# Kernel optimization log

Measured on AMD Instinct MI355X. Metric: run time of the kernel, lower is better.

## Reference

```python
import jax, jax.numpy as jnp
import numpy as np

N = 20000       # nodes
E = 640000      # edges (before self-loops)
F_IN = 128      # num_features
H = 128         # hidden channels (both GAT layers)
C = 40          # num_classes
NEG_SLOPE = 0.2  # PyG GATConv default


def _glorot(key, shape):
    fan = sum(shape)
    return jax.random.normal(key, shape, dtype=jnp.float32) * jnp.sqrt(2.0 / fan)


def setup_inputs() -> dict:
    key = jax.random.key(0)
    ks = jax.random.split(key, 12)
    x = jax.random.normal(ks[0], (N, F_IN), dtype=jnp.float32)
    edge_index = jax.random.randint(ks[1], (2, E), 0, N, dtype=jnp.int64)
    return {
        "x": x,
        "edge_index": edge_index,
        # GATConv layer 1 (heads=1): lin weight, att_src, att_dst, bias
        "W1": _glorot(ks[2], (F_IN, H)),
        "a1_src": _glorot(ks[3], (H,)),
        "a1_dst": _glorot(ks[4], (H,)),
        "b1": jnp.zeros((H,), dtype=jnp.float32),
        # GATConv layer 2
        "W2": _glorot(ks[5], (H, H)),
        "a2_src": _glorot(ks[6], (H,)),
        "a2_dst": _glorot(ks[7], (H,)),
        "b2": jnp.zeros((H,), dtype=jnp.float32),
        # final linear classifier
        "Wl": _glorot(ks[8], (H, C)),
        "bl": jnp.zeros((C,), dtype=jnp.float32),
    }


def gat_conv(x, src, dst, W, a_src, a_dst, b):
    """PyG GATConv, heads=1, concat=True, negative_slope=0.2 (self-loops already in edge list)."""
    h = x @ W                                   # [N, H]
    alpha_src = h @ a_src                       # [N]
    alpha_dst = h @ a_dst                       # [N]
    e = jax.nn.leaky_relu(alpha_src[src] + alpha_dst[dst], NEG_SLOPE)  # [E']
    # numerically stable softmax over incoming edges per destination node
    m = jax.ops.segment_max(e, dst, num_segments=N)        # [N]
    ex = jnp.exp(e - m[dst])                                # [E']
    den = jax.ops.segment_sum(ex, dst, num_segments=N)      # [N]
    alpha = ex / den[dst]                                   # [E']
    out = jax.ops.segment_sum(h[src] * alpha[:, None], dst, num_segments=N)  # [N, H]
    return out + b


def reference(x, edge_index, W1, a1_src, a1_dst, b1, W2, a2_src, a2_dst, b2, Wl, bl):
    # GATConv adds self-loops by default
    loops = jnp.arange(N, dtype=edge_index.dtype)
    src = jnp.concatenate([edge_index[0], loops])
    dst = jnp.concatenate([edge_index[1], loops])
    h = jax.nn.relu(gat_conv(x, src, dst, W1, a1_src, a1_dst, b1))
    h = jax.nn.relu(gat_conv(h, src, dst, W2, a2_src, a2_dst, b2))
    # F.dropout with training=False is identity (eval mode)
    return h @ Wl + bl
```

## Files before the change

kernel.cpp:

```cpp
#include <hip/hip_runtime.h>
#include <hip/hip_fp16.h>
#include <math.h>

#define NNODES 20000
#define NEDGE  640000
#define ETOT   (NEDGE + NNODES)
#define FDIM   128
#define CDIM   40
#define NEG    0.2f

#define NB     157
#define BCAP   6144
#define EPB    2048
#define NBLKA  ((ETOT + EPB - 1) / EPB)

__device__ __forceinline__ float lrelu(float v) { return v >= 0.f ? v : NEG * v; }

__device__ __forceinline__ void edge_sd(const int* __restrict__ ei, int e, int& s, int& d) {
    if (e < NEDGE) { s = ei[e]; d = ei[NEDGE + e]; }
    else { int n = e - NEDGE; s = n; d = n; }
}

__global__ __launch_bounds__(256) void zero_bcnt_k(int* bcnt) {
    if (threadIdx.x < NB) bcnt[threadIdx.x] = 0;
}

__global__ __launch_bounds__(256) void bucketA_k(const int* __restrict__ ei,
                                                 int* __restrict__ bcnt,
                                                 unsigned* __restrict__ bbuf) {
    __shared__ int lhist[NB];
    __shared__ int lbase[NB];
    __shared__ int lcur[NB];
    __shared__ unsigned stash[EPB];
    const int t = threadIdx.x;
    const int e0 = blockIdx.x * EPB;
    for (int i = t; i < NB; i += 256) { lhist[i] = 0; lcur[i] = 0; }
    __syncthreads();
    #pragma unroll
    for (int j = 0; j < EPB / 256; ++j) {
        int e = e0 + j * 256 + t;
        unsigned pk = 0xFFFFFFFFu;
        if (e < ETOT) {
            int s, d; edge_sd(ei, e, s, d);
            atomicAdd(&lhist[d >> 7], 1);
            pk = ((unsigned)(d >> 7) << 22) | ((unsigned)(d & 127) << 15) | (unsigned)s;
        }
        stash[j * 256 + t] = pk;
    }
    __syncthreads();
    for (int i = t; i < NB; i += 256) {
        int c = lhist[i];
        lbase[i] = c ? atomicAdd(&bcnt[i], c) : 0;
    }
    __syncthreads();
    #pragma unroll
    for (int j = 0; j < EPB / 256; ++j) {
        unsigned pk = stash[j * 256 + t];
        if (pk != 0xFFFFFFFFu) {
            int b = pk >> 22;
            int r = atomicAdd(&lcur[b], 1);
            bbuf[(size_t)b * BCAP + lbase[b] + r] = pk & 0x3FFFFFu;
        }
    }
}

__global__ __launch_bounds__(1024) void bucketB_k(const int* __restrict__ bcnt,
                                                  const unsigned* __restrict__ bbuf,
                                                  int* __restrict__ start,
                                                  int* __restrict__ ssrc) {
    __shared__ int pre[NB];
    __shared__ int hist[128], hstart[128], hcur[128];
    __shared__ unsigned st[BCAP];
    const int t = threadIdx.x;
    const int b = blockIdx.x;
    if (t < NB) pre[t] = bcnt[t];
    if (t < 128) hist[t] = 0;
    __syncthreads();
    for (int off = 1; off < NB; off <<= 1) {
        int v = 0;
        if (t < NB && t >= off) v = pre[t - off];
        __syncthreads();
        if (t < NB) pre[t] += v;
        __syncthreads();
    }
    const int n0 = bcnt[b];
    const int n = n0 < BCAP ? n0 : BCAP;
    const int base = (b == 0) ? 0 : pre[b - 1];
    for (int i = t; i < n; i += 1024) {
        unsigned pk = bbuf[(size_t)b * BCAP + i];
        st[i] = pk;
        atomicAdd(&hist[(pk >> 15) & 127], 1);
    }
    __syncthreads();
    if (t < 128) hstart[t] = hist[t];
    __syncthreads();
    for (int off = 1; off < 128; off <<= 1) {
        int v = 0;
        if (t < 128 && t >= off) v = hstart[t - off];
        __syncthreads();
        if (t < 128) hstart[t] += v;
        __syncthreads();
    }
    if (t < 128) { int ex = hstart[t] - hist[t]; hstart[t] = ex; hcur[t] = ex; }
    __syncthreads();
    const int d0 = b << 7;
    const int ndst = min(128, NNODES - d0);
    if (t < ndst) start[d0 + t] = base + hstart[t];
    if (b == 0 && t == 0) start[NNODES] = ETOT;
    for (int i = t; i < n; i += 1024) {
        unsigned pk = st[i];
        int r = atomicAdd(&hcur[(pk >> 15) & 127], 1);
        ssrc[base + r] = (int)(pk & 0x7FFFu);
    }
}

__global__ __launch_bounds__(256) void gemm_alphas_k(const float* __restrict__ X,
                                                     const float* __restrict__ W,
                                                     const float* __restrict__ a_src,
                                                     const float* __restrict__ a_dst,
                                                     __half* __restrict__ H16,
                                                     float* __restrict__ asrc,
                                                     float* __restrict__ adst) {
    __shared__ float Ws[FDIM * FDIM];
    for (int i = threadIdx.x; i < FDIM * FDIM; i += 256) Ws[i] = W[i];
    __syncthreads();
    const int rsub = threadIdx.x >> 5;
    const int c4 = (threadIdx.x & 31) * 4;
    const int row0 = blockIdx.x * 32 + rsub * 4;
    const float* xr = X + (size_t)row0 * FDIM;
    const float4 as4 = *(const float4*)(a_src + c4);
    const float4 ad4 = *(const float4*)(a_dst + c4);
    float4 acc[4];
    #pragma unroll
    for (int r = 0; r < 4; ++r) acc[r] = make_float4(0.f, 0.f, 0.f, 0.f);
    #pragma unroll 4
    for (int k = 0; k < FDIM; k += 4) {
        const float4 w0 = *(const float4*)(Ws + (k + 0) * FDIM + c4);
        const float4 w1 = *(const float4*)(Ws + (k + 1) * FDIM + c4);
        const float4 w2 = *(const float4*)(Ws + (k + 2) * FDIM + c4);
        const float4 w3 = *(const float4*)(Ws + (k + 3) * FDIM + c4);
        #pragma unroll
        for (int r = 0; r < 4; ++r) {
            const float4 xv = *(const float4*)(xr + (size_t)r * FDIM + k);
            acc[r].x = fmaf(xv.x, w0.x, acc[r].x); acc[r].y = fmaf(xv.x, w0.y, acc[r].y);
            acc[r].z = fmaf(xv.x, w0.z, acc[r].z); acc[r].w = fmaf(xv.x, w0.w, acc[r].w);
            acc[r].x = fmaf(xv.y, w1.x, acc[r].x); acc[r].y = fmaf(xv.y, w1.y, acc[r].y);
            acc[r].z = fmaf(xv.y, w1.z, acc[r].z); acc[r].w = fmaf(xv.y, w1.w, acc[r].w);
            acc[r].x = fmaf(xv.z, w2.x, acc[r].x); acc[r].y = fmaf(xv.z, w2.y, acc[r].y);
            acc[r].z = fmaf(xv.z, w2.z, acc[r].z); acc[r].w = fmaf(xv.z, w2.w, acc[r].w);
            acc[r].x = fmaf(xv.w, w3.x, acc[r].x); acc[r].y = fmaf(xv.w, w3.y, acc[r].y);
            acc[r].z = fmaf(xv.w, w3.z, acc[r].z); acc[r].w = fmaf(xv.w, w3.w, acc[r].w);
        }
    }
    #pragma unroll
    for (int r = 0; r < 4; ++r) {
        union { __half2 h[2]; float2 f; } u;
        u.h[0] = __floats2half2_rn(acc[r].x, acc[r].y);
        u.h[1] = __floats2half2_rn(acc[r].z, acc[r].w);
        *(float2*)(H16 + (size_t)(row0 + r) * FDIM + c4) = u.f;
        float ps = acc[r].x * as4.x + acc[r].y * as4.y + acc[r].z * as4.z + acc[r].w * as4.w;
        float pd = acc[r].x * ad4.x + acc[r].y * ad4.y + acc[r].z * ad4.z + acc[r].w * ad4.w;
        #pragma unroll
        for (int off = 16; off; off >>= 1) {
            ps += __shfl_down(ps, off, 32);
            pd += __shfl_down(pd, off, 32);
        }
        if ((threadIdx.x & 31) == 0) { asrc[row0 + r] = ps; adst[row0 + r] = pd; }
    }
}

__global__ __launch_bounds__(256) void gat_agg_k(const __half* __restrict__ H16,
                                                 const float* __restrict__ asrc,
                                                 const float* __restrict__ adst,
                                                 const int* __restrict__ start,
                                                 const int* __restrict__ ssrc,
                                                 const float* __restrict__ bias,
                                                 float* __restrict__ out) {
    int w = (blockIdx.x * 256 + threadIdx.x) >> 6;
    int lane = threadIdx.x & 63;
    if (w >= NNODES) return;
    const float ad = adst[w];
    const int lo = start[w], hi = start[w + 1];
    float den = 0.f, a0 = 0.f, a1 = 0.f;
    int i = lo;
    for (; i + 8 <= hi; i += 8) {
        int s[8];
        #pragma unroll
        for (int j = 0; j < 8; ++j) s[j] = ssrc[i + j];
        float p[8];
        __half2 hv[8];
        #pragma unroll
        for (int j = 0; j < 8; ++j) {
            p[j] = __expf(lrelu(asrc[s[j]] + ad));
            hv[j] = *(const __half2*)(H16 + (size_t)s[j] * FDIM + lane * 2);
        }
        #pragma unroll
        for (int j = 0; j < 8; ++j) {
            const float2 f = __half22float2(hv[j]);
            den += p[j];
            a0 = fmaf(p[j], f.x, a0);
            a1 = fmaf(p[j], f.y, a1);
        }
    }
    for (; i < hi; ++i) {
        const int s = ssrc[i];
        const float p = __expf(lrelu(asrc[s] + ad));
        const float2 f = __half22float2(*(const __half2*)(H16 + (size_t)s * FDIM + lane * 2));
        den += p;
        a0 = fmaf(p, f.x, a0);
        a1 = fmaf(p, f.y, a1);
    }
    const float inv = 1.f / den;
    const float v0 = fmaf(a0, inv, bias[lane * 2]);
    const float v1 = fmaf(a1, inv, bias[lane * 2 + 1]);
    float* o = out + (size_t)w * FDIM + lane * 2;
    o[0] = v0 > 0.f ? v0 : 0.f;
    o[1] = v1 > 0.f ? v1 : 0.f;
}

__global__ __launch_bounds__(320) void classifier_k(const float* __restrict__ H,
                                                    const float* __restrict__ Wl,
                                                    const float* __restrict__ bl,
                                                    float* __restrict__ out) {
    __shared__ float Ws[FDIM * CDIM];
    __shared__ float bs[CDIM];
    for (int i = threadIdx.x; i < FDIM * CDIM; i += 320) Ws[i] = Wl[i];
    if (threadIdx.x < CDIM) bs[threadIdx.x] = bl[threadIdx.x];
    __syncthreads();
    const int cq = threadIdx.x % 10;
    const int rsub = threadIdx.x / 10;
    const int c4 = cq * 4;
    const int row0 = blockIdx.x * 64 + rsub * 2;
    const int r0 = min(row0, NNODES - 1);
    const int r1 = min(row0 + 1, NNODES - 1);
    const float* x0 = H + (size_t)r0 * FDIM;
    const float* x1 = H + (size_t)r1 * FDIM;
    float4 a0 = make_float4(0.f, 0.f, 0.f, 0.f);
    float4 a1 = make_float4(0.f, 0.f, 0.f, 0.f);
    #pragma unroll 4
    for (int k = 0; k < FDIM; k += 4) {
        const float4 w0 = *(const float4*)(Ws + (k + 0) * CDIM + c4);
        const float4 w1 = *(const float4*)(Ws + (k + 1) * CDIM + c4);
        const float4 w2 = *(const float4*)(Ws + (k + 2) * CDIM + c4);
        const float4 w3 = *(const float4*)(Ws + (k + 3) * CDIM + c4);
        const float4 v0 = *(const float4*)(x0 + k);
        const float4 v1 = *(const float4*)(x1 + k);
        a0.x = fmaf(v0.x, w0.x, a0.x); a0.y = fmaf(v0.x, w0.y, a0.y);
        a0.z = fmaf(v0.x, w0.z, a0.z); a0.w = fmaf(v0.x, w0.w, a0.w);
        a0.x = fmaf(v0.y, w1.x, a0.x); a0.y = fmaf(v0.y, w1.y, a0.y);
        a0.z = fmaf(v0.y, w1.z, a0.z); a0.w = fmaf(v0.y, w1.w, a0.w);
        a0.x = fmaf(v0.z, w2.x, a0.x); a0.y = fmaf(v0.z, w2.y, a0.y);
        a0.z = fmaf(v0.z, w2.z, a0.z); a0.w = fmaf(v0.z, w2.w, a0.w);
        a0.x = fmaf(v0.w, w3.x, a0.x); a0.y = fmaf(v0.w, w3.y, a0.y);
        a0.z = fmaf(v0.w, w3.z, a0.z); a0.w = fmaf(v0.w, w3.w, a0.w);
        a1.x = fmaf(v1.x, w0.x, a1.x); a1.y = fmaf(v1.x, w0.y, a1.y);
        a1.z = fmaf(v1.x, w0.z, a1.z); a1.w = fmaf(v1.x, w0.w, a1.w);
        a1.x = fmaf(v1.y, w1.x, a1.x); a1.y = fmaf(v1.y, w1.y, a1.y);
        a1.z = fmaf(v1.y, w1.z, a1.z); a1.w = fmaf(v1.y, w1.w, a1.w);
        a1.x = fmaf(v1.z, w2.x, a1.x); a1.y = fmaf(v1.z, w2.y, a1.y);
        a1.z = fmaf(v1.z, w2.z, a1.z); a1.w = fmaf(v1.z, w2.w, a1.w);
        a1.x = fmaf(v1.w, w3.x, a1.x); a1.y = fmaf(v1.w, w3.y, a1.y);
        a1.z = fmaf(v1.w, w3.z, a1.z); a1.w = fmaf(v1.w, w3.w, a1.w);
    }
    const float4 bb = *(const float4*)(bs + c4);
    a0.x += bb.x; a0.y += bb.y; a0.z += bb.z; a0.w += bb.w;
    a1.x += bb.x; a1.y += bb.y; a1.z += bb.z; a1.w += bb.w;
    if (row0 < NNODES)     *(float4*)(out + (size_t)row0 * CDIM + c4) = a0;
    if (row0 + 1 < NNODES) *(float4*)(out + (size_t)(row0 + 1) * CDIM + c4) = a1;
}

extern "C" void kernel_launch(void* const* d_in, const int* in_sizes, int n_in,
                              void* d_out, int out_size, void* d_ws, size_t ws_size,
                              hipStream_t stream) {
    const float* x   = (const float*)d_in[0];
    const int*   ei  = (const int*)d_in[1];
    const float* W1  = (const float*)d_in[2];
    const float* a1s = (const float*)d_in[3];
    const float* a1d = (const float*)d_in[4];
    const float* b1  = (const float*)d_in[5];
    const float* W2  = (const float*)d_in[6];
    const float* a2s = (const float*)d_in[7];
    const float* a2d = (const float*)d_in[8];
    const float* b2  = (const float*)d_in[9];
    const float* Wl  = (const float*)d_in[10];
    const float* bl  = (const float*)d_in[11];
    float* out = (float*)d_out;

    char* ws = (char*)d_ws;
    __half*   H16   = (__half*)(ws);
    float*    bufB  = (float*)(ws + 5120000);
    float*    asrc  = (float*)(ws + 15360000);
    float*    adst  = (float*)(ws + 15440000);
    int*      start = (int*)  (ws + 15520000);
    int*      ssrc  = (int*)  (ws + 15600004);
    int*      bcnt  = (int*)  (ws + 18240004);
    unsigned* bbuf  = (unsigned*)(ws + 18240632);

    zero_bcnt_k<<<1, 256, 0, stream>>>(bcnt);
    bucketA_k<<<NBLKA, 256, 0, stream>>>(ei, bcnt, bbuf);
    bucketB_k<<<NB, 1024, 0, stream>>>(bcnt, bbuf, start, ssrc);

    gemm_alphas_k<<<625, 256, 0, stream>>>(x, W1, a1s, a1d, H16, asrc, adst);
    gat_agg_k<<<5000, 256, 0, stream>>>(H16, asrc, adst, start, ssrc, b1, bufB);

    gemm_alphas_k<<<625, 256, 0, stream>>>(bufB, W2, a2s, a2d, H16, asrc, adst);
    gat_agg_k<<<5000, 256, 0, stream>>>(H16, asrc, adst, start, ssrc, b2, bufB);

    classifier_k<<<313, 320, 0, stream>>>(bufB, Wl, bl, out);
}
```

Before: 139.3 us.

## Precompute per-edge attention weights in a separate kernel before aggregation

Packs source and destination into one word per sorted edge and adds an edge-parallel kernel that computes exp(leaky_relu(asrc+adst)) once per edge into a buffer reused from the bucket scratch. In the aggregation kernel this replaces 64 redundant per-lane asrc gathers and expf calls with plain loads, and the unroll is widened from 8 to 16 with a 4-wide tail. The cost is an extra launch per layer plus writing and reading an edge-sized float array.

```diff
diff --git a/kernel.cpp b/kernel.cpp
--- a/kernel.cpp
+++ b/kernel.cpp
@@ -67,7 +67,7 @@
 __global__ __launch_bounds__(1024) void bucketB_k(const int* __restrict__ bcnt,
                                                   const unsigned* __restrict__ bbuf,
                                                   int* __restrict__ start,
-                                                  int* __restrict__ ssrc) {
+                                                  unsigned* __restrict__ ssd) {
     __shared__ int pre[NB];
     __shared__ int hist[128], hstart[128], hcur[128];
     __shared__ unsigned st[BCAP];
@@ -107,11 +107,24 @@
     const int ndst = min(128, NNODES - d0);
     if (t < ndst) start[d0 + t] = base + hstart[t];
     if (b == 0 && t == 0) start[NNODES] = ETOT;
+    const unsigned dofs = (unsigned)d0 << 15;
     for (int i = t; i < n; i += 1024) {
         unsigned pk = st[i];
         int r = atomicAdd(&hcur[(pk >> 15) & 127], 1);
-        ssrc[base + r] = (int)(pk & 0x7FFFu);
-    }
+        ssd[base + r] = pk + dofs;
+    }
+}
+
+__global__ __launch_bounds__(256) void edge_p_k(const unsigned* __restrict__ ssd,
+                                                const float* __restrict__ asrc,
+                                                const float* __restrict__ adst,
+                                                float* __restrict__ p) {
+    int i = blockIdx.x * 256 + threadIdx.x;
+    if (i >= ETOT) return;
+    const unsigned v = ssd[i];
+    const int s = (int)(v & 0x7FFFu);
+    const int d = (int)(v >> 15);
+    p[i] = __expf(lrelu(asrc[s] + adst[d]));
 }
 
 __global__ __launch_bounds__(256) void gemm_alphas_k(const float* __restrict__ X,
@@ -170,50 +183,68 @@
 }
 
 __global__ __launch_bounds__(256) void gat_agg_k(const __half* __restrict__ H16,
-                                                 const float* __restrict__ asrc,
-                                                 const float* __restrict__ adst,
+                                                 const float* __restrict__ p,
+                                                 const unsigned* __restrict__ ssd,
                                                  const int* __restrict__ start,
-                                                 const int* __restrict__ ssrc,
                                                  const float* __restrict__ bias,
                                                  float* __restrict__ out) {
     int w = (blockIdx.x * 256 + threadIdx.x) >> 6;
-    int lane = threadIdx.x & 63;
     if (w >= NNODES) return;
-    const float ad = adst[w];
+    const int lane = threadIdx.x & 63;
     const int lo = start[w], hi = start[w + 1];
+    const size_t coff = (size_t)lane * 2;
     float den = 0.f, a0 = 0.f, a1 = 0.f;
     int i = lo;
-    for (; i + 8 <= hi; i += 8) {
-        int s[8];
-        #pragma unroll
-        for (int j = 0; j < 8; ++j) s[j] = ssrc[i + j];
-        float p[8];
-        __half2 hv[8];
-        #pragma unroll
-        for (int j = 0; j < 8; ++j) {
-            p[j] = __expf(lrelu(asrc[s[j]] + ad));
-            hv[j] = *(const __half2*)(H16 + (size_t)s[j] * FDIM + lane * 2);
-        }
-        #pragma unroll
-        for (int j = 0; j < 8; ++j) {
+    for (; i + 16 <= hi; i += 16) {
+        int s[16]; float pp[16];
+        #pragma unroll
+        for (int j = 0; j < 16; ++j) {
+            s[j] = (int)(ssd[i + j] & 0x7FFFu);
+            pp[j] = p[i + j];
+        }
+        __half2 hv[16];
+        #pragma unroll
+        for (int j = 0; j < 16; ++j)
+            hv[j] = *(const __half2*)(H16 + (size_t)s[j] * FDIM + coff);
+        #pragma unroll
+        for (int j = 0; j < 16; ++j) {
             const float2 f = __half22float2(hv[j]);
-            den += p[j];
-            a0 = fmaf(p[j], f.x, a0);
-            a1 = fmaf(p[j], f.y, a1);
+            den += pp[j];
+            a0 = fmaf(pp[j], f.x, a0);
+            a1 = fmaf(pp[j], f.y, a1);
+        }
+    }
+    for (; i + 4 <= hi; i += 4) {
+        int s[4]; float pp[4];
+        #pragma unroll
+        for (int j = 0; j < 4; ++j) {
+            s[j] = (int)(ssd[i + j] & 0x7FFFu);
+            pp[j] = p[i + j];
+        }
+        __half2 hv[4];
+        #pragma unroll
+        for (int j = 0; j < 4; ++j)
+            hv[j] = *(const __half2*)(H16 + (size_t)s[j] * FDIM + coff);
+        #pragma unroll
+        for (int j = 0; j < 4; ++j) {
+            const float2 f = __half22float2(hv[j]);
+            den += pp[j];
+            a0 = fmaf(pp[j], f.x, a0);
+            a1 = fmaf(pp[j], f.y, a1);
         }
     }
     for (; i < hi; ++i) {
-        const int s = ssrc[i];
-        const float p = __expf(lrelu(asrc[s] + ad));
-        const float2 f = __half22float2(*(const __half2*)(H16 + (size_t)s * FDIM + lane * 2));
-        den += p;
-        a0 = fmaf(p, f.x, a0);
-        a1 = fmaf(p, f.y, a1);
+        const int s = (int)(ssd[i] & 0x7FFFu);
+        const float pj = p[i];
+        const float2 f = __half22float2(*(const __half2*)(H16 + (size_t)s * FDIM + coff));
+        den += pj;
+        a0 = fmaf(pj, f.x, a0);
+        a1 = fmaf(pj, f.y, a1);
     }
     const float inv = 1.f / den;
     const float v0 = fmaf(a0, inv, bias[lane * 2]);
     const float v1 = fmaf(a1, inv, bias[lane * 2 + 1]);
-    float* o = out + (size_t)w * FDIM + lane * 2;
+    float* o = out + (size_t)w * FDIM + coff;
     o[0] = v0 > 0.f ? v0 : 0.f;
     o[1] = v1 > 0.f ? v1 : 0.f;
 }
@@ -292,19 +323,24 @@
     float*    asrc  = (float*)(ws + 15360000);
     float*    adst  = (float*)(ws + 15440000);
     int*      start = (int*)  (ws + 15520000);
-    int*      ssrc  = (int*)  (ws + 15600004);
+    unsigned* ssd   = (unsigned*)(ws + 15600004);
     int*      bcnt  = (int*)  (ws + 18240004);
     unsigned* bbuf  = (unsigned*)(ws + 18240632);
+    float*    pbuf  = (float*)bbuf;
+
+    const int gEdge = (ETOT + 255) / 256;
 
     zero_bcnt_k<<<1, 256, 0, stream>>>(bcnt);
     bucketA_k<<<NBLKA, 256, 0, stream>>>(ei, bcnt, bbuf);
-    bucketB_k<<<NB, 1024, 0, stream>>>(bcnt, bbuf, start, ssrc);
+    bucketB_k<<<NB, 1024, 0, stream>>>(bcnt, bbuf, start, ssd);
 
     gemm_alphas_k<<<625, 256, 0, stream>>>(x, W1, a1s, a1d, H16, asrc, adst);
-    gat_agg_k<<<5000, 256, 0, stream>>>(H16, asrc, adst, start, ssrc, b1, bufB);
+    edge_p_k<<<gEdge, 256, 0, stream>>>(ssd, asrc, adst, pbuf);
+    gat_agg_k<<<5000, 256, 0, stream>>>(H16, pbuf, ssd, start, b1, bufB);
 
     gemm_alphas_k<<<625, 256, 0, stream>>>(bufB, W2, a2s, a2d, H16, asrc, adst);
-    gat_agg_k<<<5000, 256, 0, stream>>>(H16, asrc, adst, start, ssrc, b2, bufB);
+    edge_p_k<<<gEdge, 256, 0, stream>>>(ssd, asrc, adst, pbuf);
+    gat_agg_k<<<5000, 256, 0, stream>>>(H16, pbuf, ssd, start, b2, bufB);
 
     classifier_k<<<313, 320, 0, stream>>>(bufB, Wl, bl, out);
 }
```

New measurement: 139.0 us. About the same (-0.2%).
